# Optimization experiments

Measured on AMD Instinct MI355X. Metric: run time of the kernel, lower is better.

The kernel has to match this reference:

```python
import jax, jax.numpy as jnp
import numpy as np

B, H, W, C = 8, 64, 64, 512
SCALING = 8
C_ = C // SCALING  # 64
N = H * W          # 4096


def setup_inputs() -> dict:
    key = jax.random.key(0)
    ks = jax.random.split(key, 8)
    scale = 1.0 / np.sqrt(C)
    x = jax.random.normal(ks[0], (B, H, W, C), dtype=jnp.float32)
    # 1x1 convs == per-pixel dense layers: weight [C_in, C_out] + bias
    Wg = jax.random.normal(ks[1], (C, C_), dtype=jnp.float32) * scale
    bg = jnp.zeros((C_,), dtype=jnp.float32)
    Wf = jax.random.normal(ks[2], (C, C_), dtype=jnp.float32) * scale
    bf = jnp.zeros((C_,), dtype=jnp.float32)
    Wh = jax.random.normal(ks[3], (C, C), dtype=jnp.float32) * scale
    bh = jnp.zeros((C,), dtype=jnp.float32)
    gamma = jnp.zeros((C,), dtype=jnp.float32)  # tf.initializers.Zeros
    return {"x": x, "Wg": Wg, "bg": bg, "Wf": Wf, "bf": bf,
            "Wh": Wh, "bh": bh, "gamma": gamma}


def reference(x, Wg, bg, Wf, bf, Wh, bh, gamma):
    b = x.shape[0]
    xf_flat = x.reshape(b, N, C)                     # [B, N, C]
    x_g = xf_flat @ Wg + bg                          # [B, N, C_]
    x_f = xf_flat @ Wf + bf                          # [B, N, C_]
    x_h = xf_flat @ Wh + bh                          # [B, N, C]
    s = jnp.einsum('bnc,bmc->bnm', x_g, x_f)         # [B, N, N]
    s = jax.nn.softmax(s, axis=-1)
    o = jnp.einsum('bnm,bmc->bnc', s, x_h)           # [B, N, C]
    o = o.reshape(b, H, W, C)
    return gamma * o + x
```

## Files before the change

### kernel.cpp

```cpp
#include <hip/hip_runtime.h>
#include <stdint.h>

using s8v  = __attribute__((ext_vector_type(8))) short;
using f4   = __attribute__((ext_vector_type(4))) float;
using u32x4 = __attribute__((ext_vector_type(4))) uint32_t;
using u32x2 = __attribute__((ext_vector_type(2))) uint32_t;
using vf4  = __attribute__((ext_vector_type(4))) float;
using i4v  = __attribute__((ext_vector_type(4))) int;

typedef unsigned short ushortT;

static __device__ __forceinline__ uint32_t bfr16(float f) {
  union { float f; uint32_t u; } v; v.f = f;
  return (v.u + 0x7FFFu + ((v.u >> 16) & 1u)) >> 16;
}
static __device__ __forceinline__ uint32_t pk2(float lo, float hi) {
  return (bfr16(hi) << 16) | (bfr16(lo) & 0xFFFFu);
}
static __device__ __forceinline__ uint32_t pk4fp8(float a, float b, float cc, float d) {
  int w = __builtin_amdgcn_cvt_pk_fp8_f32(a, b, 0, false);
  w = __builtin_amdgcn_cvt_pk_fp8_f32(cc, d, w, true);
  return (uint32_t)w;
}
static __device__ __forceinline__ void gl16(const void* g, void* l) {
  __builtin_amdgcn_global_load_lds((const __attribute__((address_space(1))) uint32_t*)g,
                                   (__attribute__((address_space(3))) uint32_t*)l, 16, 0, 0);
}

#define MFMA_BF16(A, B, C) __builtin_amdgcn_mfma_f32_16x16x32_bf16((A), (B), (C), 0, 0, 0)
#define MFMA_FP8(A, B, C)  __builtin_amdgcn_mfma_f32_16x16x32_fp8_fp8((A), (B), (C), 0, 0, 0)

__global__ __launch_bounds__(64) void kprep(const float* __restrict__ Wg,
                                            const float* __restrict__ Wf,
                                            const float* __restrict__ Wh,
                                            ushortT* __restrict__ Wt) {
  const int cIdx = blockIdx.x;
  const int t = threadIdx.x;
  const float* src; int co, ldc;
  if (cIdx < 64)       { src = Wg; co = cIdx;       ldc = 64;  }
  else if (cIdx < 128) { src = Wf; co = cIdx - 64;  ldc = 64;  }
  else                 { src = Wh; co = cIdx - 128; ldc = 512; }
#pragma unroll
  for (int kk = 0; kk < 8; ++kk) {
    int k = kk * 64 + t;
    Wt[(size_t)cIdx * 512 + k] = (ushortT)bfr16(src[(size_t)k * ldc + co]);
  }
}

__global__ __launch_bounds__(256) void kproj(const float* __restrict__ x,
                                             const ushortT* __restrict__ Wt,
                                             const float* __restrict__ bg,
                                             const float* __restrict__ bfv,
                                             const float* __restrict__ bh,
                                             ushortT* __restrict__ Q,
                                             ushortT* __restrict__ K,
                                             uint8_t* __restrict__ V8) {
  __shared__ ushortT Al[64 * 64];
  __shared__ ushortT Bl[64 * 64];

  const int tid = threadIdx.x;
  const int w = tid >> 6, l = tid & 63, h = l >> 4, c = l & 15;
  const int ct = blockIdx.x, rt = blockIdx.y;
  const int row0 = rt * 64;

  f4 acc[4];
#pragma unroll
  for (int j = 0; j < 4; ++j) acc[j] = (f4){0.f, 0.f, 0.f, 0.f};

  const int arow = tid >> 2, aseg = tid & 3;
  const float* xrow = x + (size_t)(row0 + arow) * 512 + aseg * 16;

  for (int kk = 0; kk < 8; ++kk) {
    const int k0 = kk * 64;
    vf4 f0 = *(const vf4*)(xrow + k0 + 0);
    vf4 f1 = *(const vf4*)(xrow + k0 + 4);
    vf4 f2 = *(const vf4*)(xrow + k0 + 8);
    vf4 f3 = *(const vf4*)(xrow + k0 + 12);
    u32x4 ch0 = { pk2(f0[0], f0[1]), pk2(f0[2], f0[3]), pk2(f1[0], f1[1]), pk2(f1[2], f1[3]) };
    u32x4 ch1 = { pk2(f2[0], f2[1]), pk2(f2[2], f2[3]), pk2(f3[0], f3[1]), pk2(f3[2], f3[3]) };
    const int sw = arow & 7;
    *(u32x4*)((char*)Al + arow * 128 + (((aseg * 2 + 0) ^ sw) * 16)) = ch0;
    *(u32x4*)((char*)Al + arow * 128 + (((aseg * 2 + 1) ^ sw) * 16)) = ch1;
#pragma unroll
    for (int j = 0; j < 2; ++j) {
      const int col = w * 16 + j * 8 + (l >> 3);
      const int c7 = l & 7;
      const ushortT* src = Wt + (size_t)(ct * 64 + col) * 512 + k0 + 8 * (c7 ^ (l >> 3));
      gl16(src, (char*)Bl + (w * 128 + j * 64) * 16);
    }
    __syncthreads();
#pragma unroll
    for (int ks = 0; ks < 2; ++ks) {
      s8v af = *(const s8v*)((char*)Al + (w * 16 + c) * 128 + (((ks * 4 + h) ^ (c & 7)) * 16));
#pragma unroll
      for (int cj = 0; cj < 4; ++cj) {
        s8v bf8 = *(const s8v*)((char*)Bl + (cj * 16 + c) * 128 + (((ks * 4 + h) ^ (c & 7)) * 16));
        acc[cj] = MFMA_BF16(af, bf8, acc[cj]);
      }
    }
    __syncthreads();
  }

  const int colbase = ct * 64;
  const float* bias = (ct == 0) ? bg : (ct == 1) ? bfv : bh;
  const int bo = (ct < 2) ? 0 : (colbase - 128);
  const int rbase = row0 + w * 16 + h * 4;
  if (ct < 2) {
    ushortT* dst = (ct == 0) ? Q : K;
#pragma unroll
    for (int cj = 0; cj < 4; ++cj) {
      const int cl = cj * 16 + c;
      const float bv = bias[cl];
#pragma unroll
      for (int r = 0; r < 4; ++r)
        dst[(size_t)(rbase + r) * 64 + cl] = (ushortT)bfr16(acc[cj][r] + bv);
    }
  } else {
    const int b = row0 >> 12;
    const int n0 = (row0 & 4095) + w * 16 + h * 4;
    const int tt = n0 >> 5, kvo = n0 & 31;
#pragma unroll
    for (int cj = 0; cj < 4; ++cj) {
      const int cl = cj * 16 + c;
      const float bv = bias[bo + cl];
      const int vcol = bo + cl;
      const uint32_t dd = pk4fp8(acc[cj][0] + bv, acc[cj][1] + bv,
                                 acc[cj][2] + bv, acc[cj][3] + bv);
      *(uint32_t*)(V8 + (((size_t)(b * 128 + tt) * 512 + vcol) * 32 + kvo)) = dd;
    }
  }
}

__global__ __launch_bounds__(512, 4) void kattn(const ushortT* __restrict__ Qg,
                                                const ushortT* __restrict__ Kg,
                                                const uint8_t* __restrict__ V8,
                                                const float* __restrict__ x,
                                                const float* __restrict__ gamma,
                                                float* __restrict__ out) {
  __shared__ __align__(16) uint32_t Pl[2][2][512];
  __shared__ __align__(16) ushortT Klds[2][64 * 64];
  __shared__ __align__(16) float alpha_s[2][64];
  __shared__ __align__(16) int   flag_s[2][4];
  __shared__ __align__(16) float lsum_s[64];

  const int tid = threadIdx.x;
  const int w = tid >> 6, l = tid & 63, h = l >> 4, c = l & 15;
  const int bb = blockIdx.x & 7, qb = blockIdx.x >> 3;
  const size_t qrow0 = (size_t)bb * 4096 + (size_t)qb * 64;

  f4 acc[4][4];
#pragma unroll
  for (int qi = 0; qi < 4; ++qi)
#pragma unroll
    for (int vj = 0; vj < 4; ++vj) acc[qi][vj] = (f4){0.f, 0.f, 0.f, 0.f};

  const ushortT* Kb = Kg + (size_t)bb * 4096 * 64;
  const uint8_t* Vb = V8 + (size_t)bb * 512 * 4096;

  const uint8_t* vptr = Vb + (size_t)(w * 64 + c) * 32 + h * 8;
  const size_t koff = (size_t)(w * 16 + (l >> 3)) * 64 + 8 * ((l & 7) ^ (l >> 3));

  s8v qf[2];
  if (w < 4) {
#pragma unroll
    for (int ks = 0; ks < 2; ++ks)
      qf[ks] = *(const s8v*)(Qg + (qrow0 + w * 16 + c) * 64 + ks * 32 + h * 8);
  }
  float m_run = -__builtin_inff();
  float l_run = 0.0f;

  auto softmax_store = [&](const f4* sc, int nb) {
    float tm = fmaxf(fmaxf(fmaxf(sc[0][0], sc[0][1]), fmaxf(sc[0][2], sc[0][3])),
                     fmaxf(fmaxf(sc[1][0], sc[1][1]), fmaxf(sc[1][2], sc[1][3])));
    tm = fmaxf(tm, fmaxf(fmaxf(fmaxf(sc[2][0], sc[2][1]), fmaxf(sc[2][2], sc[2][3])),
                         fmaxf(fmaxf(sc[3][0], sc[3][1]), fmaxf(sc[3][2], sc[3][3]))));
    const unsigned long long bal = __ballot(tm > m_run + 4.0f);
    float al = 1.0f;
    if (bal) {
      tm = fmaxf(tm, __shfl_xor(tm, 16));
      tm = fmaxf(tm, __shfl_xor(tm, 32));
      const float mn = fmaxf(m_run, tm);
      al = __expf(m_run - mn);
      m_run = mn;
    }
    float ps = 0.0f;
#pragma unroll
    for (int j = 0; j < 4; ++j) {
      const float p0 = __expf(sc[j][0] - m_run), p1 = __expf(sc[j][1] - m_run);
      const float p2 = __expf(sc[j][2] - m_run), p3 = __expf(sc[j][3] - m_run);
      ps += (p0 + p1) + (p2 + p3);
      const uint32_t pw = pk4fp8(p0, p1, p2, p3);
      const int s = j >> 1;
      const int hc = 2 * (j & 1) + (h >> 1);
      Pl[nb][s][(w * 64 + c + 16 * hc) * 2 + (h & 1)] = pw;
    }
    l_run = l_run * al + ps;
    if (bal && h == 0) alpha_s[nb][w * 16 + c] = al;
    if (l == 0) flag_s[nb][w] = bal ? 1 : 0;
  };

  auto produce_lds = [&](int kb, int nb) {
    f4 sc[4];
#pragma unroll
    for (int j = 0; j < 4; ++j) sc[j] = (f4){0.f, 0.f, 0.f, 0.f};
    const char* kbp = (const char*)Klds[kb];
    __builtin_amdgcn_s_setprio(1);
#pragma unroll
    for (int j = 0; j < 4; ++j) {
#pragma unroll
      for (int ks = 0; ks < 2; ++ks) {
        s8v kf = *(const s8v*)(kbp + (size_t)(j * 16 + c) * 128 +
                               (((ks * 4 + h) ^ (c & 7)) * 16));
        sc[j] = MFMA_BF16(kf, qf[ks], sc[j]);
      }
    }
    __builtin_amdgcn_s_setprio(0);
    softmax_store(sc, nb);
  };

  if (w < 4) {
    f4 sc[4];
#pragma unroll
    for (int j = 0; j < 4; ++j) sc[j] = (f4){0.f, 0.f, 0.f, 0.f};
#pragma unroll
    for (int j = 0; j < 4; ++j) {
#pragma unroll
      for (int ks = 0; ks < 2; ++ks) {
        s8v kf = *(const s8v*)(Kb + (size_t)(j * 16 + c) * 64 + ks * 32 + h * 8);
        sc[j] = MFMA_BF16(kf, qf[ks], sc[j]);
      }
    }
    softmax_store(sc, 0);
    gl16(Kb + 4096 + koff, (char*)Klds[1] + w * 2048);
    gl16(Kb + 4096 + koff + 512, (char*)Klds[1] + w * 2048 + 1024);
  }
  asm volatile("s_waitcnt vmcnt(0) lgkmcnt(0)" ::: "memory");
  __builtin_amdgcn_s_barrier();

  for (int t = 0; t < 64; ++t) {
    const int cur = t & 1;
    long paA[4], paB[4];
#pragma unroll
    for (int qi = 0; qi < 4; ++qi) {
      paA[qi] = *(const long*)&Pl[cur][0][(qi * 64 + l) * 2];
      paB[qi] = *(const long*)&Pl[cur][1][(qi * 64 + l) * 2];
    }
    i4v fl = *(const i4v*)&flag_s[cur][0];
    if (w < 4 && t < 62) {
      const ushortT* ks_src = Kb + (size_t)(t + 2) * 4096 + koff;
      gl16(ks_src, (char*)Klds[cur] + w * 2048);
      gl16(ks_src + 512, (char*)Klds[cur] + w * 2048 + 1024);
    }
#pragma unroll
    for (int qi = 0; qi < 4; ++qi) {
      if (fl[qi]) {
        f4 a4 = *(const f4*)&alpha_s[cur][qi * 16 + h * 4];
#pragma unroll
        for (int vj = 0; vj < 4; ++vj)
#pragma unroll
          for (int r = 0; r < 4; ++r) acc[qi][vj][r] *= a4[r];
      }
    }
#pragma unroll
    for (int vj = 0; vj < 4; ++vj) {
      const long vf0 = *(const long*)(vptr + vj * 512);
      const long vf1 = *(const long*)(vptr + 16384 + vj * 512);
      __builtin_amdgcn_s_setprio(1);
#pragma unroll
      for (int qi = 0; qi < 4; ++qi) {
        acc[qi][vj] = MFMA_FP8(paA[qi], vf0, acc[qi][vj]);
        acc[qi][vj] = MFMA_FP8(paB[qi], vf1, acc[qi][vj]);
      }
      __builtin_amdgcn_s_setprio(0);
    }
    vptr += 32768;
    if (t < 63) {
      if (w < 4) produce_lds(cur ^ 1, cur ^ 1);
      asm volatile("s_waitcnt vmcnt(0) lgkmcnt(0)" ::: "memory");
      __builtin_amdgcn_s_barrier();
    }
  }

  l_run += __shfl_xor(l_run, 16);
  l_run += __shfl_xor(l_run, 32);
  if (w < 4 && h == 0) lsum_s[w * 16 + c] = l_run;
  __syncthreads();
#pragma unroll
  for (int qi = 0; qi < 4; ++qi) {
    f4 l4 = *(const f4*)(&lsum_s[qi * 16 + h * 4]);
    f4 rl;
#pragma unroll
    for (int r = 0; r < 4; ++r) rl[r] = 1.0f / l4[r];
#pragma unroll
    for (int vj = 0; vj < 4; ++vj) {
      const int colg = w * 64 + vj * 16 + c;
      const float gm = gamma[colg];
#pragma unroll
      for (int r = 0; r < 4; ++r) {
        const size_t idx = (qrow0 + qi * 16 + h * 4 + r) * 512 + colg;
        out[idx] = gm * (acc[qi][vj][r] * rl[r]) + x[idx];
      }
    }
  }
}

extern "C" void kernel_launch(void* const* d_in, const int* in_sizes, int n_in,
                              void* d_out, int out_size, void* d_ws, size_t ws_size,
                              hipStream_t stream) {
  const float* x     = (const float*)d_in[0];
  const float* Wg    = (const float*)d_in[1];
  const float* bg    = (const float*)d_in[2];
  const float* Wf    = (const float*)d_in[3];
  const float* bfv   = (const float*)d_in[4];
  const float* Wh    = (const float*)d_in[5];
  const float* bh    = (const float*)d_in[6];
  const float* gamma = (const float*)d_in[7];
  float* out = (float*)d_out;
  char* ws = (char*)d_ws;

  ushortT* Q  = (ushortT*)(ws);
  ushortT* K  = (ushortT*)(ws + ((size_t)4 << 20));
  uint8_t* V8 = (uint8_t*)(ws + ((size_t)8 << 20));
  ushortT* Wt = (ushortT*)(ws + ((size_t)40 << 20));

  kprep<<<dim3(640), dim3(64), 0, stream>>>(Wg, Wf, Wh, Wt);
  kproj<<<dim3(10, 512), dim3(256), 0, stream>>>(x, Wt, bg, bfv, bh, Q, K, V8);
  kattn<<<dim3(512), dim3(512), 0, stream>>>(Q, K, V8, x, gamma, out);
}
```

Measured before the change: 251.9 us.

## Enlarge projection tiles to 128x128 and fold log2e into Q for exp2 softmax

The projection GEMM moves from 64x64 to 128x128 output tiles, with each wave computing a 64x64 sub-tile through a 4x4 MFMA accumulator grid. This raises reuse of A and B fragments loaded from LDS and halves how often x is re-read across column tiles, at the cost of more accumulator registers. Q is pre-scaled by log2e so the attention softmax can use exp2f in place of __expf, and the rescale threshold is adjusted to match the base-2 scale.

```diff
diff --git a/kernel.cpp b/kernel.cpp
--- a/kernel.cpp
+++ b/kernel.cpp
@@ -9,6 +9,8 @@
 using i4v  = __attribute__((ext_vector_type(4))) int;
 
 typedef unsigned short ushortT;
+
+#define LOG2E 1.4426950408889634f
 
 static __device__ __forceinline__ uint32_t bfr16(float f) {
   union { float f; uint32_t u; } v; v.f = f;
@@ -55,78 +57,94 @@
                                              ushortT* __restrict__ Q,
                                              ushortT* __restrict__ K,
                                              uint8_t* __restrict__ V8) {
-  __shared__ ushortT Al[64 * 64];
-  __shared__ ushortT Bl[64 * 64];
+  __shared__ ushortT Al[128 * 64];
+  __shared__ ushortT Bl[128 * 64];
 
   const int tid = threadIdx.x;
   const int w = tid >> 6, l = tid & 63, h = l >> 4, c = l & 15;
+  const int wr = w >> 1, wc = w & 1;
   const int ct = blockIdx.x, rt = blockIdx.y;
-  const int row0 = rt * 64;
-
-  f4 acc[4];
-#pragma unroll
-  for (int j = 0; j < 4; ++j) acc[j] = (f4){0.f, 0.f, 0.f, 0.f};
-
-  const int arow = tid >> 2, aseg = tid & 3;
-  const float* xrow = x + (size_t)(row0 + arow) * 512 + aseg * 16;
+  const int row0 = rt * 128;
+
+  f4 acc[4][4];
+#pragma unroll
+  for (int m = 0; m < 4; ++m)
+#pragma unroll
+    for (int n = 0; n < 4; ++n) acc[m][n] = (f4){0.f, 0.f, 0.f, 0.f};
+
+  const int arow = tid >> 1, ahalf = tid & 1;
+  const float* xrow = x + (size_t)(row0 + arow) * 512 + ahalf * 32;
+  const int asw = arow & 7;
 
   for (int kk = 0; kk < 8; ++kk) {
     const int k0 = kk * 64;
-    vf4 f0 = *(const vf4*)(xrow + k0 + 0);
-    vf4 f1 = *(const vf4*)(xrow + k0 + 4);
-    vf4 f2 = *(const vf4*)(xrow + k0 + 8);
-    vf4 f3 = *(const vf4*)(xrow + k0 + 12);
-    u32x4 ch0 = { pk2(f0[0], f0[1]), pk2(f0[2], f0[3]), pk2(f1[0], f1[1]), pk2(f1[2], f1[3]) };
-    u32x4 ch1 = { pk2(f2[0], f2[1]), pk2(f2[2], f2[3]), pk2(f3[0], f3[1]), pk2(f3[2], f3[3]) };
-    const int sw = arow & 7;
-    *(u32x4*)((char*)Al + arow * 128 + (((aseg * 2 + 0) ^ sw) * 16)) = ch0;
-    *(u32x4*)((char*)Al + arow * 128 + (((aseg * 2 + 1) ^ sw) * 16)) = ch1;
-#pragma unroll
-    for (int j = 0; j < 2; ++j) {
-      const int col = w * 16 + j * 8 + (l >> 3);
-      const int c7 = l & 7;
-      const ushortT* src = Wt + (size_t)(ct * 64 + col) * 512 + k0 + 8 * (c7 ^ (l >> 3));
-      gl16(src, (char*)Bl + (w * 128 + j * 64) * 16);
+    vf4 f[8];
+#pragma unroll
+    for (int i = 0; i < 8; ++i) f[i] = *(const vf4*)(xrow + k0 + i * 4);
+#pragma unroll
+    for (int j = 0; j < 4; ++j) {
+      u32x4 ch = { pk2(f[2*j][0], f[2*j][1]),   pk2(f[2*j][2], f[2*j][3]),
+                   pk2(f[2*j+1][0], f[2*j+1][1]), pk2(f[2*j+1][2], f[2*j+1][3]) };
+      *(u32x4*)((char*)Al + arow * 128 + (((ahalf * 4 + j) ^ asw) * 16)) = ch;
+    }
+#pragma unroll
+    for (int i = 0; i < 4; ++i) {
+      const int col = w * 32 + i * 8 + (l >> 3);
+      const ushortT* src = Wt + (size_t)(ct * 128 + col) * 512 + k0 +
+                           8 * ((l & 7) ^ (l >> 3));
+      gl16(src, (char*)Bl + (w * 4 + i) * 1024);
     }
     __syncthreads();
 #pragma unroll
     for (int ks = 0; ks < 2; ++ks) {
-      s8v af = *(const s8v*)((char*)Al + (w * 16 + c) * 128 + (((ks * 4 + h) ^ (c & 7)) * 16));
-#pragma unroll
-      for (int cj = 0; cj < 4; ++cj) {
-        s8v bf8 = *(const s8v*)((char*)Bl + (cj * 16 + c) * 128 + (((ks * 4 + h) ^ (c & 7)) * 16));
-        acc[cj] = MFMA_BF16(af, bf8, acc[cj]);
-      }
+      s8v a[4], b[4];
+#pragma unroll
+      for (int m = 0; m < 4; ++m)
+        a[m] = *(const s8v*)((char*)Al + (size_t)(wr * 64 + m * 16 + c) * 128 +
+                             (((ks * 4 + h) ^ (c & 7)) * 16));
+#pragma unroll
+      for (int n = 0; n < 4; ++n)
+        b[n] = *(const s8v*)((char*)Bl + (size_t)(wc * 64 + n * 16 + c) * 128 +
+                             (((ks * 4 + h) ^ (c & 7)) * 16));
+#pragma unroll
+      for (int m = 0; m < 4; ++m)
+#pragma unroll
+        for (int n = 0; n < 4; ++n)
+          acc[m][n] = MFMA_BF16(a[m], b[n], acc[m][n]);
     }
     __syncthreads();
   }
 
-  const int colbase = ct * 64;
-  const float* bias = (ct == 0) ? bg : (ct == 1) ? bfv : bh;
-  const int bo = (ct < 2) ? 0 : (colbase - 128);
-  const int rbase = row0 + w * 16 + h * 4;
-  if (ct < 2) {
-    ushortT* dst = (ct == 0) ? Q : K;
-#pragma unroll
-    for (int cj = 0; cj < 4; ++cj) {
-      const int cl = cj * 16 + c;
-      const float bv = bias[cl];
-#pragma unroll
-      for (int r = 0; r < 4; ++r)
-        dst[(size_t)(rbase + r) * 64 + cl] = (ushortT)bfr16(acc[cj][r] + bv);
+  if (ct == 0) {
+    ushortT* dst = (wc == 0) ? Q : K;
+    const float* bias = (wc == 0) ? bg : bfv;
+    const float scl = (wc == 0) ? LOG2E : 1.0f;
+#pragma unroll
+    for (int n = 0; n < 4; ++n) {
+      const int col = n * 16 + c;
+      const float bv = bias[col];
+#pragma unroll
+      for (int m = 0; m < 4; ++m) {
+        const int grow = row0 + wr * 64 + m * 16 + h * 4;
+#pragma unroll
+        for (int r = 0; r < 4; ++r)
+          dst[(size_t)(grow + r) * 64 + col] = (ushortT)bfr16((acc[m][n][r] + bv) * scl);
+      }
     }
   } else {
     const int b = row0 >> 12;
-    const int n0 = (row0 & 4095) + w * 16 + h * 4;
-    const int tt = n0 >> 5, kvo = n0 & 31;
-#pragma unroll
-    for (int cj = 0; cj < 4; ++cj) {
-      const int cl = cj * 16 + c;
-      const float bv = bias[bo + cl];
-      const int vcol = bo + cl;
-      const uint32_t dd = pk4fp8(acc[cj][0] + bv, acc[cj][1] + bv,
-                                 acc[cj][2] + bv, acc[cj][3] + bv);
-      *(uint32_t*)(V8 + (((size_t)(b * 128 + tt) * 512 + vcol) * 32 + kvo)) = dd;
+#pragma unroll
+    for (int n = 0; n < 4; ++n) {
+      const int vcol = ct * 128 + wc * 64 + n * 16 + c - 128;
+      const float bv = bh[vcol];
+#pragma unroll
+      for (int m = 0; m < 4; ++m) {
+        const int n0 = (row0 & 4095) + wr * 64 + m * 16 + h * 4;
+        const int tt = n0 >> 5, kvo = n0 & 31;
+        const uint32_t dd = pk4fp8(acc[m][n][0] + bv, acc[m][n][1] + bv,
+                                   acc[m][n][2] + bv, acc[m][n][3] + bv);
+        *(uint32_t*)(V8 + (((size_t)(b * 128 + tt) * 512 + vcol) * 32 + kvo)) = dd;
+      }
     }
   }
 }
@@ -174,20 +192,20 @@
                      fmaxf(fmaxf(sc[1][0], sc[1][1]), fmaxf(sc[1][2], sc[1][3])));
     tm = fmaxf(tm, fmaxf(fmaxf(fmaxf(sc[2][0], sc[2][1]), fmaxf(sc[2][2], sc[2][3])),
                          fmaxf(fmaxf(sc[3][0], sc[3][1]), fmaxf(sc[3][2], sc[3][3]))));
-    const unsigned long long bal = __ballot(tm > m_run + 4.0f);
+    const unsigned long long bal = __ballot(tm > m_run + 5.77f);
     float al = 1.0f;
     if (bal) {
       tm = fmaxf(tm, __shfl_xor(tm, 16));
       tm = fmaxf(tm, __shfl_xor(tm, 32));
       const float mn = fmaxf(m_run, tm);
-      al = __expf(m_run - mn);
+      al = exp2f(m_run - mn);
       m_run = mn;
     }
     float ps = 0.0f;
 #pragma unroll
     for (int j = 0; j < 4; ++j) {
-      const float p0 = __expf(sc[j][0] - m_run), p1 = __expf(sc[j][1] - m_run);
-      const float p2 = __expf(sc[j][2] - m_run), p3 = __expf(sc[j][3] - m_run);
+      const float p0 = exp2f(sc[j][0] - m_run), p1 = exp2f(sc[j][1] - m_run);
+      const float p2 = exp2f(sc[j][2] - m_run), p3 = exp2f(sc[j][3] - m_run);
       ps += (p0 + p1) + (p2 + p3);
       const uint32_t pw = pk4fp8(p0, p1, p2, p3);
       const int s = j >> 1;
@@ -324,6 +342,6 @@
   ushortT* Wt = (ushortT*)(ws + ((size_t)40 << 20));
 
   kprep<<<dim3(640), dim3(64), 0, stream>>>(Wg, Wf, Wh, Wt);
-  kproj<<<dim3(10, 512), dim3(256), 0, stream>>>(x, Wt, bg, bfv, bh, Q, K, V8);
+  kproj<<<dim3(5, 256), dim3(256), 0, stream>>>(x, Wt, bg, bfv, bh, Q, K, V8);
   kattn<<<dim3(512), dim3(512), 0, stream>>>(Q, K, V8, x, gamma, out);
 }
```

New measurement: 246.0 us. -2.3%, faster.
